# Performance work log

Hardware: AMD Instinct MI355X
Metric: run time of the kernel (lower is better)

## Reference

```python
import jax, jax.numpy as jnp
import numpy as np

N = 8192
F_IN = 128
D = 128
NEG_SLOPE = 0.2  # cfg.negativeslope (standard GAT value)
MASK_FILL = -9e15


def setup_inputs() -> dict:
    key = jax.random.key(0)
    k1, k2, k3, k4 = jax.random.split(key, 4)
    A = jax.random.randint(k1, (N, N), 0, 2, dtype=jnp.int32)
    X = jax.random.normal(k2, (N, F_IN), dtype=jnp.float32)
    # glorot init for Ws, xavier_uniform(gain=1.414) for a
    lim_w = float(np.sqrt(6.0 / (F_IN + D)))
    Ws = jax.random.uniform(k3, (F_IN, D), minval=-lim_w, maxval=lim_w, dtype=jnp.float32)
    lim_a = 1.414 * float(np.sqrt(6.0 / (2 * D + 1)))
    a = jax.random.uniform(k4, (2 * D, 1), minval=-lim_a, maxval=lim_a, dtype=jnp.float32)
    return {"A": A, "X": X, "Ws": Ws, "a": a}


def reference(A, X, Ws, a):
    # Wh: [N, D]
    Wh = X @ Ws
    d = Wh.shape[-1]
    # additive attention: e_ij = leaky_relu(Wh_i . a1 + Wh_j . a2)
    e1 = Wh @ a[:d]          # [N, 1]
    e2 = Wh @ a[d:]          # [N, 1]
    e = jax.nn.leaky_relu(e1 + e2.T, negative_slope=NEG_SLOPE)  # [N, N]
    e = jnp.where(A > 0, e, MASK_FILL)
    attn = jax.nn.softmax(e, axis=1)  # row-wise over neighbors
    H = attn @ Wh            # [N, D]
    return H
```

## Files before the change

### kernel.cpp

```cpp
#include <hip/hip_runtime.h>
#include <hip/hip_bf16.h>

#define NN 8192
#define DD 128

typedef __attribute__((ext_vector_type(8))) short short8;
typedef __attribute__((ext_vector_type(4))) float f32x4;
typedef __attribute__((ext_vector_type(4))) int i32x4;
typedef unsigned int u32;

__device__ __forceinline__ ushort f2bf(float f) {
    __hip_bfloat16 h = __float2bfloat16(f);
    return *(ushort*)&h;
}

__device__ __forceinline__ void async_ld16(const void* g, void* l) {
    __builtin_amdgcn_global_load_lds(
        (const __attribute__((address_space(1))) u32*)g,
        (__attribute__((address_space(3))) u32*)l, 16, 0, 0);
}

__global__ __launch_bounds__(256) void k12_gemm(const float* __restrict__ X,
                                                const float* __restrict__ Ws,
                                                const float* __restrict__ a,
                                                ushort* __restrict__ WhT,
                                                float* __restrict__ C1,
                                                float* __restrict__ C1s,
                                                float2* __restrict__ E2) {
    __shared__ float lWs[128 * 132];
    __shared__ float lX[32 * 132];
    __shared__ ushort lT2[128 * 32];
    __shared__ float la[256];
    int t = threadIdx.x, bx = blockIdx.x;
    la[t] = a[t];
    const float4* Ws4 = (const float4*)Ws;
    const float4* X4 = (const float4*)X;
    for (int j = 0; j < 16; ++j) {
        int u = j * 256 + t;
        int k = u >> 5, c4 = u & 31;
        *(float4*)&lWs[k * 132 + c4 * 4] = Ws4[u];
    }
    for (int j = 0; j < 4; ++j) {
        int u = j * 256 + t;
        int r = u >> 5, c4 = u & 31;
        *(float4*)&lX[r * 132 + c4 * 4] = X4[bx * 1024 + u];
    }
    __syncthreads();
    int r0 = (t >> 5) * 4, c0 = (t & 31) * 4;
    float acc[4][4];
#pragma unroll
    for (int i = 0; i < 4; ++i)
#pragma unroll
        for (int j = 0; j < 4; ++j) acc[i][j] = 0.f;
#pragma unroll 4
    for (int k = 0; k < 128; ++k) {
        float4 wv = *(const float4*)&lWs[k * 132 + c0];
        float x0 = lX[(r0 + 0) * 132 + k];
        float x1 = lX[(r0 + 1) * 132 + k];
        float x2 = lX[(r0 + 2) * 132 + k];
        float x3 = lX[(r0 + 3) * 132 + k];
#pragma unroll
        for (int j = 0; j < 4; ++j) {
            acc[0][j] += x0 * ((const float*)&wv)[j];
            acc[1][j] += x1 * ((const float*)&wv)[j];
            acc[2][j] += x2 * ((const float*)&wv)[j];
            acc[3][j] += x3 * ((const float*)&wv)[j];
        }
    }
#pragma unroll
    for (int i = 0; i < 4; ++i)
#pragma unroll
        for (int j = 0; j < 4; ++j)
            lT2[(c0 + j) * 32 + r0 + i] = f2bf(acc[i][j]);
    float p1[4], p2[4];
#pragma unroll
    for (int i = 0; i < 4; ++i) {
        p1[i] = 0.f; p2[i] = 0.f;
#pragma unroll
        for (int j = 0; j < 4; ++j) {
            p1[i] += acc[i][j] * la[c0 + j];
            p2[i] += acc[i][j] * la[128 + c0 + j];
        }
    }
#pragma unroll
    for (int m = 1; m < 32; m <<= 1) {
#pragma unroll
        for (int i = 0; i < 4; ++i) {
            p1[i] += __shfl_xor(p1[i], m);
            p2[i] += __shfl_xor(p2[i], m);
        }
    }
    if ((t & 31) == 0) {
#pragma unroll
        for (int i = 0; i < 4; ++i) {
            int row = bx * 32 + r0 + i;
            C1[row]  = __expf(p1[i]);
            C1s[row] = __expf(0.2f * p1[i]);
            E2[row]  = make_float2(__expf(p2[i]), __expf(0.2f * p2[i]));
        }
    }
    __syncthreads();
    {
        int d = t >> 1, hf = t & 1;
        uint4* dst = (uint4*)&WhT[(size_t)d * NN + bx * 32 + hf * 16];
        const uint4* src = (const uint4*)&lT2[d * 32 + hf * 16];
        dst[0] = src[0];
        dst[1] = src[1];
    }
}

#define PACK4(b, v, sh)                                     \
    b |= (u32)((v).x & 1) << (sh);                          \
    b |= (u32)((v).y & 1) << ((sh) + 1);                    \
    b |= (u32)((v).z & 1) << ((sh) + 2);                    \
    b |= (u32)((v).w & 1) << ((sh) + 3);

__global__ __launch_bounds__(512, 2) void k3_main(
    const int* __restrict__ A, const ushort* __restrict__ WhT,
    const float* __restrict__ C1, const float* __restrict__ C1s,
    const float2* __restrict__ E2,
    float* __restrict__ Hp, float* __restrict__ Lp) {

    __shared__ __align__(16) char lB[131072];
    __shared__ __align__(16) char lE[4096];

    int tid = threadIdx.x;
    int lane = tid & 63;
    int w = tid >> 6;
    int n = lane & 15;
    int kg = lane >> 4;

    int bx = blockIdx.x;
    int kb = blockIdx.y;
    int rb = bx * 256 + w * 32;

    float c1_0 = C1[rb + n],      c1s_0 = C1s[rb + n];
    float c1_1 = C1[rb + 16 + n], c1s_1 = C1s[rb + 16 + n];

    const int* pA0 = A + (size_t)(rb + n) * NN + (size_t)kb * 512 + kg * 8;
    const int* pA1 = pA0 + (size_t)16 * NN;

    i32x4 ar[8];
    u32 a_cur0, a_cur1;

#pragma unroll
    for (int tp = 0; tp < 2; ++tp) {
        ar[tp * 2 + 0]     = __builtin_nontemporal_load((const i32x4*)(pA0 + tp * 32));
        ar[tp * 2 + 1]     = __builtin_nontemporal_load((const i32x4*)(pA0 + tp * 32 + 4));
        ar[4 + tp * 2 + 0] = __builtin_nontemporal_load((const i32x4*)(pA1 + tp * 32));
        ar[4 + tp * 2 + 1] = __builtin_nontemporal_load((const i32x4*)(pA1 + tp * 32 + 4));
    }

#pragma unroll
    for (int i = 0; i < 16; ++i) {
        int p = w + i * 8;
        int kt = p >> 4, tp = (p >> 3) & 1, c = p & 7;
        const ushort* src = WhT + (size_t)(c * 16 + n) * NN +
                            (size_t)kb * 512 + kt * 64 + tp * 32 + kg * 8;
        async_ld16(src, lB + p * 1024 + lane * 16);
    }
    if (w == 0)
#pragma unroll
        for (int i = 0; i < 4; ++i)
            async_ld16((const char*)(E2 + (size_t)kb * 512) + (i * 64 + lane) * 16,
                       lE + (i * 64 + lane) * 16);

    {
        u32 b0 = 0, b1 = 0;
#pragma unroll
        for (int tp = 0; tp < 2; ++tp) {
            PACK4(b0, ar[tp * 2 + 0], tp * 8);
            PACK4(b0, ar[tp * 2 + 1], tp * 8 + 4);
            PACK4(b1, ar[4 + tp * 2 + 0], tp * 8);
            PACK4(b1, ar[4 + tp * 2 + 1], tp * 8 + 4);
        }
        a_cur0 = b0; a_cur1 = b1;
    }

    short8 ones;
#pragma unroll
    for (int j = 0; j < 8; ++j) ones[j] = (short)0x3F80;

    f32x4 acc0[8], acc1[8];
#pragma unroll
    for (int c = 0; c < 8; ++c) {
        acc0[c] = (f32x4){0.f, 0.f, 0.f, 0.f};
        acc1[c] = (f32x4){0.f, 0.f, 0.f, 0.f};
    }
    f32x4 accl0 = (f32x4){0.f, 0.f, 0.f, 0.f};
    f32x4 accl1 = (f32x4){0.f, 0.f, 0.f, 0.f};

    __syncthreads();

    for (int kt = 0; kt < 8; ++kt) {
        if (kt < 7) {
#pragma unroll
            for (int tp = 0; tp < 2; ++tp) {
                ar[tp * 2 + 0]     = __builtin_nontemporal_load((const i32x4*)(pA0 + (kt + 1) * 64 + tp * 32));
                ar[tp * 2 + 1]     = __builtin_nontemporal_load((const i32x4*)(pA0 + (kt + 1) * 64 + tp * 32 + 4));
                ar[4 + tp * 2 + 0] = __builtin_nontemporal_load((const i32x4*)(pA1 + (kt + 1) * 64 + tp * 32));
                ar[4 + tp * 2 + 1] = __builtin_nontemporal_load((const i32x4*)(pA1 + (kt + 1) * 64 + tp * 32 + 4));
            }
        }
#pragma unroll
        for (int tp = 0; tp < 2; ++tp) {
            const float4* ev = (const float4*)((const float*)lE +
                                               (kt * 64 + tp * 32 + kg * 8) * 2);
            float pe[16];
            *(float4*)(pe + 0)  = ev[0];
            *(float4*)(pe + 4)  = ev[1];
            *(float4*)(pe + 8)  = ev[2];
            *(float4*)(pe + 12) = ev[3];
            u32 ab0 = (a_cur0 >> (tp * 8)) & 0xffu;
            u32 ab1 = (a_cur1 >> (tp * 8)) & 0xffu;
            short8 af0, af1;
#pragma unroll
            for (int u = 0; u < 8; ++u) {
                float w0 = fmaxf(c1_0 * pe[2 * u], c1s_0 * pe[2 * u + 1]);
                float w1 = fmaxf(c1_1 * pe[2 * u], c1s_1 * pe[2 * u + 1]);
                af0[u] = ((ab0 >> u) & 1u) ? (short)f2bf(w0) : (short)0;
                af1[u] = ((ab1 >> u) & 1u) ? (short)f2bf(w1) : (short)0;
            }
            const short8* bb = (const short8*)(lB + (kt * 16 + tp * 8) * 1024);
#pragma unroll
            for (int c = 0; c < 8; ++c) {
                short8 bf = bb[c * 64 + lane];
                acc0[c] = __builtin_amdgcn_mfma_f32_16x16x32_bf16(af0, bf, acc0[c], 0, 0, 0);
                acc1[c] = __builtin_amdgcn_mfma_f32_16x16x32_bf16(af1, bf, acc1[c], 0, 0, 0);
            }
            accl0 = __builtin_amdgcn_mfma_f32_16x16x32_bf16(af0, ones, accl0, 0, 0, 0);
            accl1 = __builtin_amdgcn_mfma_f32_16x16x32_bf16(af1, ones, accl1, 0, 0, 0);
        }
        if (kt < 7) {
            u32 b0 = 0, b1 = 0;
#pragma unroll
            for (int tp = 0; tp < 2; ++tp) {
                PACK4(b0, ar[tp * 2 + 0], tp * 8);
                PACK4(b0, ar[tp * 2 + 1], tp * 8 + 4);
                PACK4(b1, ar[4 + tp * 2 + 0], tp * 8);
                PACK4(b1, ar[4 + tp * 2 + 1], tp * 8 + 4);
            }
            a_cur0 = b0; a_cur1 = b1;
        }
    }

    float* Hpb = Hp + (size_t)kb * (NN * DD);
#pragma unroll
    for (int c = 0; c < 8; ++c)
#pragma unroll
        for (int r = 0; r < 4; ++r) {
            Hpb[(size_t)(rb + kg * 4 + r) * DD + c * 16 + n]      = acc0[c][r];
            Hpb[(size_t)(rb + 16 + kg * 4 + r) * DD + c * 16 + n] = acc1[c][r];
        }
    if (n == 0) {
        float* Lpb = Lp + (size_t)kb * NN;
#pragma unroll
        for (int r = 0; r < 4; ++r) {
            Lpb[rb + kg * 4 + r]      = accl0[r];
            Lpb[rb + 16 + kg * 4 + r] = accl1[r];
        }
    }
}

__global__ void k4_final(const float* __restrict__ Hp, const float* __restrict__ Lp,
                         float* __restrict__ out) {
    int g = blockIdx.x * 256 + threadIdx.x;
    int i = g >> 5;
    float4 sv = make_float4(0.f, 0.f, 0.f, 0.f);
    float l = 0.f;
#pragma unroll
    for (int kb = 0; kb < 16; ++kb) {
        float4 v = *(const float4*)(Hp + (size_t)kb * (NN * DD) + (size_t)g * 4);
        sv.x += v.x; sv.y += v.y; sv.z += v.z; sv.w += v.w;
        l += Lp[(size_t)kb * NN + i];
    }
    float r = 1.f / l;
    *(float4*)(out + (size_t)g * 4) = make_float4(sv.x * r, sv.y * r, sv.z * r, sv.w * r);
}

extern "C" void kernel_launch(void* const* d_in, const int* in_sizes, int n_in,
                              void* d_out, int out_size, void* d_ws, size_t ws_size,
                              hipStream_t stream) {
    const int*   A  = (const int*)d_in[0];
    const float* X  = (const float*)d_in[1];
    const float* Ws = (const float*)d_in[2];
    const float* a  = (const float*)d_in[3];
    float* out = (float*)d_out;

    char* ws = (char*)d_ws;
    ushort* WhT = (ushort*)(ws);
    float*  C1  = (float*)(ws + (2u << 20));
    float*  C1s = (float*)(ws + (2u << 20) + (32u << 10));
    float2* E2  = (float2*)(ws + (2u << 20) + (64u << 10));
    float*  Hp  = (float*)(ws + (3u << 20));
    float*  Lp  = (float*)(ws + (67u << 20));

    k12_gemm<<<256, 256, 0, stream>>>(X, Ws, a, WhT, C1, C1s, E2);
    k3_main<<<dim3(32, 16), 512, 0, stream>>>(A, WhT, C1, C1s, E2, Hp, Lp);
    k4_final<<<1024, 256, 0, stream>>>(Hp, Lp, out);
}
```

Before: 412.1 us.

## Prepack adjacency mask into LDS bitmasks via wave ballot before main loop

The per-iteration strided 16-byte loads of A, which fed bit packing in the MFMA loop, are replaced by an upfront pass. Each wave reads its 32 rows of the A tile with fully coalesced per-lane int loads, builds 64-bit masks with ballot, and stores them to a new LDS buffer. The main loop then reads its mask bytes from LDS. This improves coalescing and drops the packing ALU work from the inner loop, but the A load is no longer overlapped with compute and adds about 18KB of LDS per block, which may hurt occupancy at two blocks per CU.

```diff
diff --git a/kernel.cpp b/kernel.cpp
--- a/kernel.cpp
+++ b/kernel.cpp
@@ -6,8 +6,8 @@
 
 typedef __attribute__((ext_vector_type(8))) short short8;
 typedef __attribute__((ext_vector_type(4))) float f32x4;
-typedef __attribute__((ext_vector_type(4))) int i32x4;
 typedef unsigned int u32;
+typedef unsigned long long u64;
 
 __device__ __forceinline__ ushort f2bf(float f) {
     __hip_bfloat16 h = __float2bfloat16(f);
@@ -109,11 +109,7 @@
     }
 }
 
-#define PACK4(b, v, sh)                                     \
-    b |= (u32)((v).x & 1) << (sh);                          \
-    b |= (u32)((v).y & 1) << ((sh) + 1);                    \
-    b |= (u32)((v).z & 1) << ((sh) + 2);                    \
-    b |= (u32)((v).w & 1) << ((sh) + 3);
+#define MROW 72
 
 __global__ __launch_bounds__(512, 2) void k3_main(
     const int* __restrict__ A, const ushort* __restrict__ WhT,
@@ -123,6 +119,7 @@
 
     __shared__ __align__(16) char lB[131072];
     __shared__ __align__(16) char lE[4096];
+    __shared__ __align__(16) char lM[256 * MROW];
 
     int tid = threadIdx.x;
     int lane = tid & 63;
@@ -136,20 +133,6 @@
 
     float c1_0 = C1[rb + n],      c1s_0 = C1s[rb + n];
     float c1_1 = C1[rb + 16 + n], c1s_1 = C1s[rb + 16 + n];
-
-    const int* pA0 = A + (size_t)(rb + n) * NN + (size_t)kb * 512 + kg * 8;
-    const int* pA1 = pA0 + (size_t)16 * NN;
-
-    i32x4 ar[8];
-    u32 a_cur0, a_cur1;
-
-#pragma unroll
-    for (int tp = 0; tp < 2; ++tp) {
-        ar[tp * 2 + 0]     = __builtin_nontemporal_load((const i32x4*)(pA0 + tp * 32));
-        ar[tp * 2 + 1]     = __builtin_nontemporal_load((const i32x4*)(pA0 + tp * 32 + 4));
-        ar[4 + tp * 2 + 0] = __builtin_nontemporal_load((const i32x4*)(pA1 + tp * 32));
-        ar[4 + tp * 2 + 1] = __builtin_nontemporal_load((const i32x4*)(pA1 + tp * 32 + 4));
-    }
 
 #pragma unroll
     for (int i = 0; i < 16; ++i) {
@@ -166,15 +149,20 @@
                        lE + (i * 64 + lane) * 16);
 
     {
-        u32 b0 = 0, b1 = 0;
-#pragma unroll
-        for (int tp = 0; tp < 2; ++tp) {
-            PACK4(b0, ar[tp * 2 + 0], tp * 8);
-            PACK4(b0, ar[tp * 2 + 1], tp * 8 + 4);
-            PACK4(b1, ar[4 + tp * 2 + 0], tp * 8);
-            PACK4(b1, ar[4 + tp * 2 + 1], tp * 8 + 4);
-        }
-        a_cur0 = b0; a_cur1 = b1;
+        const int* pA = A + (size_t)(rb) * NN + (size_t)kb * 512 + lane;
+        for (int r8 = 0; r8 < 32; ++r8) {
+            const int* rp = pA + (size_t)r8 * NN;
+            int v[8];
+#pragma unroll
+            for (int c = 0; c < 8; ++c)
+                v[c] = __builtin_nontemporal_load(rp + c * 64);
+#pragma unroll
+            for (int c = 0; c < 8; ++c) {
+                u64 m = __ballot(v[c] != 0);
+                if (lane == 0)
+                    *(u64*)(lM + (w * 32 + r8) * MROW + c * 8) = m;
+            }
+        }
     }
 
     short8 ones;
@@ -192,16 +180,12 @@
 
     __syncthreads();
 
+    const char* mrow0 = lM + (w * 32 + n) * MROW;
+    const char* mrow1 = lM + (w * 32 + 16 + n) * MROW;
+
     for (int kt = 0; kt < 8; ++kt) {
-        if (kt < 7) {
-#pragma unroll
-            for (int tp = 0; tp < 2; ++tp) {
-                ar[tp * 2 + 0]     = __builtin_nontemporal_load((const i32x4*)(pA0 + (kt + 1) * 64 + tp * 32));
-                ar[tp * 2 + 1]     = __builtin_nontemporal_load((const i32x4*)(pA0 + (kt + 1) * 64 + tp * 32 + 4));
-                ar[4 + tp * 2 + 0] = __builtin_nontemporal_load((const i32x4*)(pA1 + (kt + 1) * 64 + tp * 32));
-                ar[4 + tp * 2 + 1] = __builtin_nontemporal_load((const i32x4*)(pA1 + (kt + 1) * 64 + tp * 32 + 4));
-            }
-        }
+        uint2 m0 = *(const uint2*)(mrow0 + kt * 8);
+        uint2 m1 = *(const uint2*)(mrow1 + kt * 8);
 #pragma unroll
         for (int tp = 0; tp < 2; ++tp) {
             const float4* ev = (const float4*)((const float*)lE +
@@ -211,8 +195,8 @@
             *(float4*)(pe + 4)  = ev[1];
             *(float4*)(pe + 8)  = ev[2];
             *(float4*)(pe + 12) = ev[3];
-            u32 ab0 = (a_cur0 >> (tp * 8)) & 0xffu;
-            u32 ab1 = (a_cur1 >> (tp * 8)) & 0xffu;
+            u32 ab0 = ((tp ? m0.y : m0.x) >> (kg * 8)) & 0xffu;
+            u32 ab1 = ((tp ? m1.y : m1.x) >> (kg * 8)) & 0xffu;
             short8 af0, af1;
 #pragma unroll
             for (int u = 0; u < 8; ++u) {
@@ -230,17 +214,6 @@
             }
             accl0 = __builtin_amdgcn_mfma_f32_16x16x32_bf16(af0, ones, accl0, 0, 0, 0);
             accl1 = __builtin_amdgcn_mfma_f32_16x16x32_bf16(af1, ones, accl1, 0, 0, 0);
-        }
-        if (kt < 7) {
-            u32 b0 = 0, b1 = 0;
-#pragma unroll
-            for (int tp = 0; tp < 2; ++tp) {
-                PACK4(b0, ar[tp * 2 + 0], tp * 8);
-                PACK4(b0, ar[tp * 2 + 1], tp * 8 + 4);
-                PACK4(b1, ar[4 + tp * 2 + 0], tp * 8);
-                PACK4(b1, ar[4 + tp * 2 + 1], tp * 8 + 4);
-            }
-            a_cur0 = b0; a_cur1 = b1;
         }
     }
 
```

Result: no change. 411.1 us (-0.2%).
